# Optimization experiments

Hardware: AMD Instinct MI355X
Metric: run time of the kernel (lower is better)

Reference implementation:

```python
import jax, jax.numpy as jnp
import numpy as np

B, L = 2048, 64          # sentence pairs, leaves per balanced binary tree
V, IN, M, HID, NC = 50000, 300, 150, 50, 5


def setup_inputs() -> dict:
    key = jax.random.key(0)
    ks = jax.random.split(key, 16)
    lin = lambda k, fi, fo: jax.random.normal(k, (fi, fo), jnp.float32) / np.sqrt(fi).astype(np.float32)
    bias = lambda k, fo: jax.random.normal(k, (fo,), jnp.float32) * 0.01
    return {
        "ltokens": jax.random.randint(ks[0], (B, L), 0, V, dtype=jnp.int32),
        "rtokens": jax.random.randint(ks[1], (B, L), 0, V, dtype=jnp.int32),
        "emb":   jax.random.normal(ks[2], (V, IN), jnp.float32),
        "Wioux": lin(ks[3], IN, 3 * M), "bioux": bias(ks[4], 3 * M),
        "Wiouh": lin(ks[5], M, 3 * M), "biouh": bias(ks[6], 3 * M),
        "Wfx":   lin(ks[7], IN, M),    "bfx":   bias(ks[8], M),
        "Wfh":   lin(ks[9], M, M),     "bfh":   bias(ks[10], M),
        "Wh":    lin(ks[11], 2 * M, HID), "bh": bias(ks[12], HID),
        "Wp":    lin(ks[13], HID, NC),    "bp": bias(ks[14], NC),
    }


def _split_iou(iou, m):
    return iou[..., :m], iou[..., m:2 * m], iou[..., 2 * m:]


def _encode(tokens, emb, Wioux, bioux, Wiouh, biouh, Wfh, bfh):
    m = Wfh.shape[0]
    x = emb[tokens]                                   # [B, L, IN]
    # Leaves: child_h = child_c = 0, so iouh contributes only its bias and fc = 0.
    iou = x @ Wioux + bioux + biouh                   # [B, L, 3M]
    i, o, u = _split_iou(iou, m)
    c = jax.nn.sigmoid(i) * jnp.tanh(u)
    h = jax.nn.sigmoid(o) * jnp.tanh(c)
    # Internal nodes level by level (inputs=None branch of node_forward).
    while h.shape[1] > 1:
        Bq, n, _ = h.shape
        ch = h.reshape(Bq, n // 2, 2, m)              # children h
        cc = c.reshape(Bq, n // 2, 2, m)              # children c
        iou = ch.sum(axis=2) @ Wiouh + biouh          # child-sum
        i, o, u = _split_iou(iou, m)
        f = jax.nn.sigmoid(ch @ Wfh + bfh)            # per-child forget gate
        c = jax.nn.sigmoid(i) * jnp.tanh(u) + (f * cc).sum(axis=2)
        h = jax.nn.sigmoid(o) * jnp.tanh(c)
    # ROOT in the original just passes its single child's state through.
    return h[:, 0]                                    # [B, M]


def reference(ltokens, rtokens, emb, Wioux, bioux, Wiouh, biouh, Wfx, bfx, Wfh, bfh, Wh, bh, Wp, bp):
    lh = _encode(ltokens, emb, Wioux, bioux, Wiouh, biouh, Wfh, bfh)
    rh = _encode(rtokens, emb, Wioux, bioux, Wiouh, biouh, Wfh, bfh)
    vec = jnp.concatenate([lh * rh, jnp.abs(lh - rh)], axis=-1)   # [B, 2M]
    mid = jax.nn.sigmoid(vec @ Wh + bh)
    return jax.nn.log_softmax(mid @ Wp + bp, axis=-1)             # [B, NC]
```

## Files before the change

kernel.cpp:

```cpp
#include <hip/hip_runtime.h>
#include <hip/hip_bf16.h>
#include <math.h>

constexpr int B_   = 2048;
constexpr int L_   = 64;
constexpr int V_   = 50000;
constexpr int IN_  = 300;
constexpr int M_   = 150;
constexpr int HID_ = 50;
constexpr int NC_  = 5;

constexpr int KP_  = 160;
constexpr int GN_  = 608;
constexpr int GNT_ = 19;
constexpr int GKC_ = 5;
constexpr int GCH_ = GN_ * 32;
constexpr int GQS_ = GN_ * 8;
constexpr int GN2_  = 640;
constexpr int GNT2_ = 10;
constexpr int GCH2_ = GN2_ * 32;
constexpr int GQS2_ = GN2_ * 8;
constexpr int LEAF_N  = 480;
constexpr int LEAF_NT = 15;
constexpr int LEAF_KC = 10;
constexpr int LEAF_CH = LEAF_N * 32;
constexpr int LEAF_QS = LEAF_N * 8;

typedef float f32x4  __attribute__((ext_vector_type(4)));
typedef short bf16x8 __attribute__((ext_vector_type(8)));
typedef short short4v __attribute__((ext_vector_type(4)));

__device__ __forceinline__ float rcp_f(float x) { return __builtin_amdgcn_rcpf(x); }
__device__ __forceinline__ float sgm(float x)   { return rcp_f(1.0f + __expf(-x)); }
__device__ __forceinline__ float tanh_f(float x){ return 1.0f - 2.0f * rcp_f(1.0f + __expf(2.0f * x)); }

__device__ __forceinline__ short f2bs(float f) {
    union { __hip_bfloat16 h; short s; } u; u.h = __float2bfloat16(f); return u.s;
}
__device__ __forceinline__ float bs2f(short s) {
    union { short s; __hip_bfloat16 h; } u; u.s = s; return __bfloat162float(u.h);
}

__device__ __forceinline__ void gl_lds16(const short* g, short* l) {
    __builtin_amdgcn_global_load_lds(
        (const __attribute__((address_space(1))) unsigned int*)g,
        (__attribute__((address_space(3))) unsigned int*)l, 16, 0, 0);
}

__global__ __launch_bounds__(256) void prep_kernel(
    const float* __restrict__ Wioux, const float* __restrict__ Wiouh,
    const float* __restrict__ Wfh, short* __restrict__ Bg,
    short* __restrict__ Bg2, short* __restrict__ Bx)
{
    const int tid = blockIdx.x * blockDim.x + threadIdx.x;
    const int nthr = gridDim.x * blockDim.x;
    const int tot1 = GKC_ * GCH_;
    for (int idx = tid; idx < tot1; idx += nthr) {
        const int kc = idx / GCH_;
        int rem = idx % GCH_;
        const int q = rem / GQS_; rem %= GQS_;
        const int n = rem / 8, j = rem % 8;
        const int k = kc * 32 + q * 8 + j;
        const int m = n >> 2, g = n & 3;
        float v = 0.0f;
        if (k < M_ && m < M_)
            v = (g < 3) ? Wiouh[k * 450 + g * 150 + m] : Wfh[k * M_ + m];
        Bg[idx] = f2bs(v);
    }
    const int tot2 = GKC_ * GCH2_;
    for (int idx = tid; idx < tot2; idx += nthr) {
        const int kc = idx / GCH2_;
        int rem = idx % GCH2_;
        const int q = rem / GQS2_; rem %= GQS2_;
        const int n = rem / 8, j = rem % 8;
        const int k = kc * 32 + q * 8 + j;
        const int m = n >> 2, g = n & 3;
        float v = 0.0f;
        if (k < M_ && m < M_)
            v = (g < 3) ? Wiouh[k * 450 + g * 150 + m] : Wfh[k * M_ + m];
        Bg2[idx] = f2bs(v);
    }
    const int tot3 = LEAF_KC * LEAF_CH;
    for (int idx = tid; idx < tot3; idx += nthr) {
        const int kc = idx / LEAF_CH;
        int rem = idx % LEAF_CH;
        const int q = rem / LEAF_QS; rem %= LEAF_QS;
        const int n = rem / 8, j = rem % 8;
        const int k = kc * 32 + q * 8 + j;
        float v = (k < IN_ && n < 450) ? Wioux[k * 450 + n] : 0.0f;
        Bx[idx] = f2bs(v);
    }
}

__global__ __launch_bounds__(512) void leaf_gemm(
    const float* __restrict__ emb, const short* __restrict__ Bx,
    const float* __restrict__ bioux, const float* __restrict__ biouh,
    short* __restrict__ LeafH, short* __restrict__ LeafC)
{
    __shared__ __align__(16) char smem[LEAF_CH * 2 + 64 * 64];
    short* Bs = (short*)smem;
    short* As = (short*)(smem + LEAF_CH * 2);
    float* Es = (float*)smem;

    const int t = threadIdx.x;
    const int row0 = blockIdx.x * 64;
    const int w = t >> 6, lane = t & 63;
    const int mt = w & 3, nt0 = (w >> 2) * LEAF_NT;
    const int lr = lane & 15, quad = lane >> 4;

    f32x4 acc[LEAF_NT];
    #pragma unroll
    for (int i = 0; i < LEAF_NT; i++) { acc[i][0] = 0; acc[i][1] = 0; acc[i][2] = 0; acc[i][3] = 0; }

    const int arow = t >> 3, apart = t & 7;
    const int av = row0 + arow;
    const int aq = apart >> 1, aj = (apart & 1) * 4;

    for (int kc = 0; kc < LEAF_KC; kc++) {
        const short* bsrc = Bx + (size_t)kc * LEAF_CH;
        #pragma unroll
        for (int i = 0; i < 3; i++)
            gl_lds16(bsrc + (i * 512 + t) * 8, Bs + (i * 512 + (t & ~63)) * 8);
        if (t < 384)
            gl_lds16(bsrc + (1536 + t) * 8, Bs + (1536 + (t & ~63)) * 8);
        {
            const int k0 = kc * 32 + apart * 4;
            float4 x = make_float4(0.f, 0.f, 0.f, 0.f);
            if (av < V_ && k0 < IN_) x = *(const float4*)&emb[(size_t)av * IN_ + k0];
            short4v s;
            s[0] = f2bs(x.x); s[1] = f2bs(x.y); s[2] = f2bs(x.z); s[3] = f2bs(x.w);
            *(short4v*)&As[aq * 512 + arow * 8 + aj] = s;
        }
        __syncthreads();
        bf16x8 a = *(const bf16x8*)&As[quad * 512 + (mt * 16 + lr) * 8];
        #pragma unroll
        for (int i = 0; i < LEAF_NT; i++) {
            bf16x8 b = *(const bf16x8*)&Bs[quad * LEAF_QS + ((nt0 + i) * 16 + lr) * 8];
            acc[i] = __builtin_amdgcn_mfma_f32_16x16x32_bf16(a, b, acc[i], 0, 0, 0);
        }
        __syncthreads();
    }

    for (int mc = 0; mc < 4; mc++) {
        if (mt == mc) {
            #pragma unroll
            for (int i = 0; i < LEAF_NT; i++) {
                const int col = (nt0 + i) * 16 + lr;
                #pragma unroll
                for (int r = 0; r < 4; r++) Es[(quad * 4 + r) * LEAF_N + col] = acc[i][r];
            }
        }
        __syncthreads();
        for (int p = t; p < 16 * KP_; p += 512) {
            const int rl = p / KP_, n = p % KP_;
            const int v = row0 + mc * 16 + rl;
            if (v < V_) {
                if (n < M_) {
                    const float i_ = Es[rl * LEAF_N + n]       + bioux[n]       + biouh[n];
                    const float o_ = Es[rl * LEAF_N + n + 150] + bioux[n + 150] + biouh[n + 150];
                    const float u_ = Es[rl * LEAF_N + n + 300] + bioux[n + 300] + biouh[n + 300];
                    const float c = sgm(i_) * tanh_f(u_);
                    const float h = sgm(o_) * tanh_f(c);
                    LeafH[(size_t)v * KP_ + n] = f2bs(h);
                    LeafC[(size_t)v * KP_ + n] = f2bs(c);
                } else {
                    LeafH[(size_t)v * KP_ + n] = 0;
                    LeafC[(size_t)v * KP_ + n] = 0;
                }
            }
        }
        __syncthreads();
    }
}

__global__ __launch_bounds__(1024) void leafGF_gemm(
    const short* __restrict__ LeafH, const short* __restrict__ LeafC,
    const short* __restrict__ Bg2, const float* __restrict__ bfh,
    short* __restrict__ LeafE)
{
    __shared__ __align__(16) char smem[GCH2_ * 2 + 4096 + KP_ * 64 * 2 + 600];
    short* Bs   = (short*)smem;
    short* As   = (short*)(smem + GCH2_ * 2);
    short* CinS = (short*)(smem + GCH2_ * 2 + 4096);
    float* bfs  = (float*)(smem + GCH2_ * 2 + 4096 + KP_ * 64 * 2);
    short* Os = (short*)smem;

    const int t = threadIdx.x;
    const int v0 = blockIdx.x * 64;
    const int w = t >> 6, lane = t & 63;
    const int mt = w & 3, nt0 = (w >> 2) * GNT2_;
    const int lr = lane & 15, quad = lane >> 4;
    const int c = lane & 15;

    if (t < 150) bfs[t] = bfh[t];
    const short* csrc = LeafC + (size_t)v0 * KP_;
    gl_lds16(csrc + t * 8, CinS + (t & ~63) * 8);
    if (t < 256)
        gl_lds16(csrc + (1024 + t) * 8, CinS + (1024 + (t & ~63)) * 8);

    f32x4 acc[GNT2_];
    #pragma unroll
    for (int i = 0; i < GNT2_; i++) { acc[i][0] = 0; acc[i][1] = 0; acc[i][2] = 0; acc[i][3] = 0; }

    const int arow = t & 63, apart = t >> 6;
    const size_t srow = (size_t)((v0 + arow < V_) ? (v0 + arow) : 0);
    const short* asrc = LeafH + srow * KP_ + apart * 8;

    for (int kc = 0; kc < GKC_; kc++) {
        const short* bsrc = Bg2 + (size_t)kc * GCH2_;
        #pragma unroll
        for (int i = 0; i < 2; i++)
            gl_lds16(bsrc + (i * 1024 + t) * 8, Bs + (i * 1024 + (t & ~63)) * 8);
        if (t < 512)
            gl_lds16(bsrc + (2048 + t) * 8, Bs + (2048 + (t & ~63)) * 8);
        if (t < 256)
            gl_lds16(asrc + kc * 32, As + (t & ~63) * 8);
        __syncthreads();
        bf16x8 a = *(const bf16x8*)&As[quad * 512 + (mt * 16 + lr) * 8];
        #pragma unroll
        for (int i = 0; i < GNT2_; i++) {
            bf16x8 b = *(const bf16x8*)&Bs[quad * GQS2_ + ((nt0 + i) * 16 + lr) * 8];
            acc[i] = __builtin_amdgcn_mfma_f32_16x16x32_bf16(a, b, acc[i], 0, 0, 0);
        }
        __syncthreads();
    }

    for (int ph = 0; ph < 2; ph++) {
        if ((mt >> 1) == ph) {
            const int rbase = 16 * (mt & 1) + 4 * quad;
            #pragma unroll
            for (int i = 0; i < GNT2_; i++) {
                const int col = (nt0 + i) * 16 + c;
                if (col < GN_) {
                    const int m = col >> 2, g = col & 3;
                    #pragma unroll
                    for (int r = 0; r < 4; r++) {
                        short ov;
                        if (g == 3) {
                            if (m < M_) {
                                const float cc = bs2f(CinS[(32 * ph + rbase + r) * KP_ + m]);
                                ov = f2bs(sgm(acc[i][r] + bfs[m]) * cc);
                            } else ov = 0;
                        } else ov = f2bs(acc[i][r]);
                        Os[(rbase + r) * GN_ + col] = ov;
                    }
                }
            }
        }
        __syncthreads();
        const int vb = v0 + 32 * ph;
        const int4* os4 = (const int4*)Os;
        for (int u = t; u < 2432; u += 1024) {
            const int row = u / 76;
            if (vb + row < V_)
                ((int4*)(LeafE + (size_t)(vb + row) * GN_))[u - row * 76] = os4[u];
        }
        __syncthreads();
    }
}

template<int CS, int TNT>
__device__ __forceinline__ void level_epilogue(
    const f32x4* acc, int mt, int nt0, int lane,
    const short* CinS, const float* bias_s, short* Hs, short* Cs)
{
    const int q = lane >> 4, c = lane & 15, g = c & 3, lb = lane & ~3;
    #pragma unroll
    for (int i = 0; i < TNT; i++) {
        const int col = (nt0 + i) * 16 + c;
        const int m = col >> 2;
        const float vA = acc[i][0] + acc[i][1];
        const float vB = acc[i][2] + acc[i][3];
        const float iA = __shfl(vA, lb), oA = __shfl(vA, lb + 1), uA = __shfl(vA, lb + 2);
        const float iB = __shfl(vB, lb), oB = __shfl(vB, lb + 1), uB = __shfl(vB, lb + 2);
        const float fA0 = __shfl(acc[i][0], lb + 3), fA1 = __shfl(acc[i][1], lb + 3);
        const float fB0 = __shfl(acc[i][2], lb + 3), fB1 = __shfl(acc[i][3], lb + 3);
        if (g < 2 && m < M_) {
            const float iv = g ? iB : iA, ov = g ? oB : oA, uv = g ? uB : uA;
            const float fl = g ? fB0 : fA0, fr = g ? fB1 : fA1;
            const int node = 8 * mt + 2 * q + g;
            const int ch = 16 * mt + 4 * q + 2 * g;
            const float cl = bs2f(CinS[ch * CS + m]);
            const float cr = bs2f(CinS[(ch + 1) * CS + m]);
            const float bf = bias_s[450 + m];
            const float cv = sgm(iv + bias_s[m]) * tanh_f(uv + bias_s[m + 300])
                           + sgm(fl + bf) * cl + sgm(fr + bf) * cr;
            const float hv = sgm(ov + bias_s[m + 150]) * tanh_f(cv);
            Hs[node * KP_ + m] = f2bs(hv);
            Cs[node * KP_ + m] = f2bs(cv);
        }
    }
}

__global__ __launch_bounds__(512, 4) void level1_fused(
    const int* __restrict__ ltok, const int* __restrict__ rtok,
    const short* __restrict__ LeafE, const short* __restrict__ Bg,
    const float* __restrict__ biouh, const float* __restrict__ bfh,
    short* __restrict__ Hout, short* __restrict__ Cout)
{
    constexpr int CS1 = 152;
    __shared__ __align__(16) char smem[GCH_ * 2 + 20480 + 64 * CS1 * 2];
    short* Bs     = (short*)smem;
    short* AsF    = (short*)(smem + GCH_ * 2);
    short* CinS   = (short*)(smem + GCH_ * 2 + 20480);
    float* bias_s = (float*)(smem + 20480);
    short* Hs = Bs;
    short* Cs = Bs + 32 * KP_;

    const int t = threadIdx.x;
    const int out0 = blockIdx.x * 32;
    const int w = t >> 6, lane = t & 63;
    const int mt = w & 3, nt0 = (w >> 2) * GNT_;
    const int lr = lane & 15, quad = lane >> 4;

    if (t < 600) bias_s[t] = (t < 450) ? biouh[t] : bfh[t - 450];
    __syncthreads();

    {
        const int row = t >> 3, qs = t & 7;
        const int gidx = blockIdx.x * 128 + 2 * row;
        const int* tsrc = (gidx < B_ * L_) ? (ltok + gidx) : (rtok + gidx - B_ * L_);
        const short* el = LeafE + (size_t)tsrc[0] * GN_;
        const short* er = LeafE + (size_t)tsrc[1] * GN_;

        union U { int4 v[2]; short s16[16]; };
        U ue, ur, uen, urn;
        ue.v[0] = *(const int4*)(el + qs * 16);
        ue.v[1] = *(const int4*)(el + qs * 16 + 8);
        ur.v[0] = *(const int4*)(er + qs * 16);
        ur.v[1] = *(const int4*)(er + qs * 16 + 8);

        #pragma unroll 1
        for (int s = 0; s < 5; s++) {
            const int Q  = qs + 8 * s;
            const int Qn = Q + 8;
            if (s < 4 && Qn < 38) {
                uen.v[0] = *(const int4*)(el + Qn * 16);
                uen.v[1] = *(const int4*)(el + Qn * 16 + 8);
                urn.v[0] = *(const int4*)(er + Qn * 16);
                urn.v[1] = *(const int4*)(er + Qn * 16 + 8);
            }
            short4v hq = {0, 0, 0, 0}, cq = {0, 0, 0, 0};
            if (Q < 38) {
                #pragma unroll
                for (int jj = 0; jj < 4; jj++) {
                    const int m = 4 * Q + jj;
                    if (m < M_) {
                        const float i_ = bs2f(ue.s16[4 * jj])     + bs2f(ur.s16[4 * jj])     + bias_s[m];
                        const float o_ = bs2f(ue.s16[4 * jj + 1]) + bs2f(ur.s16[4 * jj + 1]) + bias_s[m + 150];
                        const float u_ = bs2f(ue.s16[4 * jj + 2]) + bs2f(ur.s16[4 * jj + 2]) + bias_s[m + 300];
                        const float fc = bs2f(ue.s16[4 * jj + 3]) + bs2f(ur.s16[4 * jj + 3]);
                        const float cv = sgm(i_) * tanh_f(u_) + fc;
                        const float hv = sgm(o_) * tanh_f(cv);
                        hq[jj] = f2bs(hv); cq[jj] = f2bs(cv);
                    }
                }
            }
            const int m0 = 4 * Q;
            const int kc = m0 >> 5, q = (m0 >> 3) & 3, j0 = m0 & 7;
            *(short4v*)&AsF[(kc * 4 + q) * 512 + row * 8 + j0] = hq;
            if (Q < 38)
                *(short4v*)&CinS[row * CS1 + m0] = cq;
            ue = uen; ur = urn;
        }
    }

    f32x4 acc[GNT_];
    #pragma unroll
    for (int i = 0; i < GNT_; i++) { acc[i][0] = 0; acc[i][1] = 0; acc[i][2] = 0; acc[i][3] = 0; }

    for (int kc = 0; kc < GKC_; kc++) {
        const short* bsrc = Bg + (size_t)kc * GCH_;
        #pragma unroll
        for (int i = 0; i < 4; i++)
            gl_lds16(bsrc + (i * 512 + t) * 8, Bs + (i * 512 + (t & ~63)) * 8);
        if (t < 384)
            gl_lds16(bsrc + (2048 + t) * 8, Bs + (2048 + (t & ~63)) * 8);
        __syncthreads();
        bf16x8 a = *(const bf16x8*)&AsF[kc * 2048 + quad * 512 + (mt * 16 + lr) * 8];
        #pragma unroll
        for (int i = 0; i < GNT_; i++) {
            bf16x8 b = *(const bf16x8*)&Bs[quad * GQS_ + ((nt0 + i) * 16 + lr) * 8];
            acc[i] = __builtin_amdgcn_mfma_f32_16x16x32_bf16(a, b, acc[i], 0, 0, 0);
        }
        __syncthreads();
    }

    if (t < 600) bias_s[t] = (t < 450) ? biouh[t] : bfh[t - 450];
    if (t < 320) { const int node = t / 10, mm = 150 + t % 10;
                   Hs[node * KP_ + mm] = 0; Cs[node * KP_ + mm] = 0; }
    __syncthreads();
    level_epilogue<CS1, GNT_>(acc, mt, nt0, lane, CinS, bias_s, Hs, Cs);
    __syncthreads();
    int4* Hg = (int4*)(Hout + (size_t)out0 * KP_);
    int4* Cg = (int4*)(Cout + (size_t)out0 * KP_);
    const int4* hs4 = (const int4*)Hs;
    const int4* cs4 = (const int4*)Cs;
    for (int u = t; u < 1280; u += 512) {
        if (u < 640) Hg[u] = hs4[u]; else Cg[u - 640] = cs4[u - 640];
    }
}

__global__ __launch_bounds__(1024) void level_gemm(
    const short* __restrict__ Hin, const short* __restrict__ Cin,
    const short* __restrict__ Bg2,
    const float* __restrict__ biouh, const float* __restrict__ bfh,
    short* __restrict__ Hout, short* __restrict__ Cout)
{
    __shared__ __align__(16) char smem[GCH2_ * 2 + 4096 + 20480 + 2400];
    short* Bs     = (short*)smem;
    short* As     = (short*)(smem + GCH2_ * 2);
    short* CinS   = (short*)(smem + GCH2_ * 2 + 4096);
    float* bias_s = (float*)(smem + GCH2_ * 2 + 4096 + 20480);
    short* Hs = Bs;
    short* Cs = Bs + 32 * KP_;

    const int t = threadIdx.x;
    const int row0 = blockIdx.x * 64, out0 = blockIdx.x * 32;
    const int w = t >> 6, lane = t & 63;
    const int mt = w & 3, nt0 = (w >> 2) * GNT2_;
    const int lr = lane & 15, quad = lane >> 4;

    if (t < 600) bias_s[t] = (t < 450) ? biouh[t] : bfh[t - 450];
    const short* csrc = Cin + (size_t)row0 * KP_;
    gl_lds16(csrc + t * 8, CinS + (t & ~63) * 8);
    if (t < 256)
        gl_lds16(csrc + (1024 + t) * 8, CinS + (1024 + (t & ~63)) * 8);

    f32x4 acc[GNT2_];
    #pragma unroll
    for (int i = 0; i < GNT2_; i++) { acc[i][0] = 0; acc[i][1] = 0; acc[i][2] = 0; acc[i][3] = 0; }

    const short* asrc = Hin + (size_t)(row0 + (t & 63)) * KP_ + (t >> 6) * 8;

    for (int kc = 0; kc < GKC_; kc++) {
        const short* bsrc = Bg2 + (size_t)kc * GCH2_;
        #pragma unroll
        for (int i = 0; i < 2; i++)
            gl_lds16(bsrc + (i * 1024 + t) * 8, Bs + (i * 1024 + (t & ~63)) * 8);
        if (t < 512)
            gl_lds16(bsrc + (2048 + t) * 8, Bs + (2048 + (t & ~63)) * 8);
        if (t < 256)
            gl_lds16(asrc + kc * 32, As + (t & ~63) * 8);
        __syncthreads();
        bf16x8 a = *(const bf16x8*)&As[quad * 512 + (mt * 16 + lr) * 8];
        #pragma unroll
        for (int i = 0; i < GNT2_; i++) {
            bf16x8 b = *(const bf16x8*)&Bs[quad * GQS2_ + ((nt0 + i) * 16 + lr) * 8];
            acc[i] = __builtin_amdgcn_mfma_f32_16x16x32_bf16(a, b, acc[i], 0, 0, 0);
        }
        __syncthreads();
    }

    if (t < 320) { const int node = t / 10, mm = 150 + t % 10;
                   Hs[node * KP_ + mm] = 0; Cs[node * KP_ + mm] = 0; }
    level_epilogue<KP_, GNT2_>(acc, mt, nt0, lane, CinS, bias_s, Hs, Cs);
    __syncthreads();
    int4* Hg = (int4*)(Hout + (size_t)out0 * KP_);
    int4* Cg = (int4*)(Cout + (size_t)out0 * KP_);
    const int4* hs4 = (const int4*)Hs;
    const int4* cs4 = (const int4*)Cs;
    for (int u = t; u < 1280; u += 1024) {
        if (u < 640) Hg[u] = hs4[u]; else Cg[u - 640] = cs4[u - 640];
    }
}

__global__ __launch_bounds__(64) void head_kernel(
    const short* __restrict__ RootH,
    const float* __restrict__ Wh, const float* __restrict__ bh,
    const float* __restrict__ Wp, const float* __restrict__ bp,
    float* __restrict__ out)
{
    __shared__ float vec[2 * M_];
    __shared__ float mid[HID_];
    __shared__ float lg[NC_];
    __shared__ float lse;

    const int b = blockIdx.x;
    const int t = threadIdx.x;
    const short* lh = RootH + (size_t)b * KP_;
    const short* rh = RootH + (size_t)(B_ + b) * KP_;

    for (int i = t; i < M_; i += 64) {
        const float a = bs2f(lh[i]), c = bs2f(rh[i]);
        vec[i]      = a * c;
        vec[M_ + i] = fabsf(a - c);
    }
    __syncthreads();

    for (int j = t; j < HID_; j += 64) {
        float acc = bh[j];
        for (int k = 0; k < 2 * M_; k++) acc += vec[k] * Wh[k * HID_ + j];
        mid[j] = sgm(acc);
    }
    __syncthreads();

    if (t < NC_) {
        float acc = bp[t];
        for (int k = 0; k < HID_; k++) acc += mid[k] * Wp[k * NC_ + t];
        lg[t] = acc;
    }
    __syncthreads();

    if (t == 0) {
        float mx = lg[0];
        for (int i = 1; i < NC_; i++) mx = fmaxf(mx, lg[i]);
        float s = 0.0f;
        for (int i = 0; i < NC_; i++) s += expf(lg[i] - mx);
        lse = mx + logf(s);
    }
    __syncthreads();

    if (t < NC_) out[b * NC_ + t] = lg[t] - lse;
}

extern "C" void kernel_launch(void* const* d_in, const int* in_sizes, int n_in,
                              void* d_out, int out_size, void* d_ws, size_t ws_size,
                              hipStream_t stream)
{
    const int*   ltok  = (const int*)d_in[0];
    const int*   rtok  = (const int*)d_in[1];
    const float* emb   = (const float*)d_in[2];
    const float* Wioux = (const float*)d_in[3];
    const float* bioux = (const float*)d_in[4];
    const float* Wiouh = (const float*)d_in[5];
    const float* biouh = (const float*)d_in[6];
    const float* Wfh   = (const float*)d_in[9];
    const float* bfh   = (const float*)d_in[10];
    const float* Wh    = (const float*)d_in[11];
    const float* bh    = (const float*)d_in[12];
    const float* Wp    = (const float*)d_in[13];
    const float* bp    = (const float*)d_in[14];
    float* out = (float*)d_out;

    char* ws = (char*)d_ws;
    size_t off = 0;
    auto carve = [&](size_t bytes) { char* p = ws + off; off += (bytes + 255) & ~(size_t)255; return p; };
    short* Bg    = (short*)carve((size_t)GKC_ * GCH_ * 2);
    short* Bg2   = (short*)carve((size_t)GKC_ * GCH2_ * 2);
    short* Bx    = (short*)carve((size_t)LEAF_KC * LEAF_CH * 2);
    short* LeafH = (short*)carve((size_t)V_ * KP_ * 2);
    short* LeafC = (short*)carve((size_t)V_ * KP_ * 2);
    short* LeafE = (short*)carve((size_t)V_ * GN_ * 2);
    short* HA    = (short*)carve((size_t)65536 * KP_ * 2);
    short* CA    = (short*)carve((size_t)65536 * KP_ * 2);
    short* HB    = (short*)carve((size_t)32768 * KP_ * 2);
    short* CB    = (short*)carve((size_t)32768 * KP_ * 2);

    hipLaunchKernelGGL(prep_kernel, dim3(128), dim3(256), 0, stream, Wioux, Wiouh, Wfh, Bg, Bg2, Bx);
    hipLaunchKernelGGL(leaf_gemm, dim3((V_ + 63) / 64), dim3(512), 0, stream,
                       emb, Bx, bioux, biouh, LeafH, LeafC);
    hipLaunchKernelGGL(leafGF_gemm, dim3((V_ + 63) / 64), dim3(1024), 0, stream,
                       LeafH, LeafC, Bg2, bfh, LeafE);
    hipLaunchKernelGGL(level1_fused, dim3(2048), dim3(512), 0, stream,
                       ltok, rtok, LeafE, Bg, biouh, bfh, HA, CA);
    hipLaunchKernelGGL(level_gemm, dim3(1024), dim3(1024), 0, stream,
                       HA, CA, Bg2, biouh, bfh, HB, CB);
    hipLaunchKernelGGL(level_gemm, dim3(512), dim3(1024), 0, stream,
                       HB, CB, Bg2, biouh, bfh, HA, CA);
    hipLaunchKernelGGL(level_gemm, dim3(256), dim3(1024), 0, stream,
                       HA, CA, Bg2, biouh, bfh, HB, CB);
    hipLaunchKernelGGL(level_gemm, dim3(128), dim3(1024), 0, stream,
                       HB, CB, Bg2, biouh, bfh, HA, CA);
    hipLaunchKernelGGL(head_kernel, dim3(B_), dim3(64), 0, stream, HA, Wh, bh, Wp, bp, out);
}
```

Baseline: 486.1 us.

## Split level1 GEMM into two N-halves and fold leaf biouh into LeafE

The level1_fused kernel now computes its 19 N-tiles in two passes of 10 and 9. After each pass the epilogue results are packed into registers, so the live accumulator set shrinks and register pressure under the 512x4 launch bounds is meant to drop. The B matrix is reloaded twice, and the shared-memory bias staging plus its barrier are removed. The i/o/u half-bias is folded into LeafE by leafGF_gemm, so the level1 prologue skips the bias adds. The cost is double B-chunk traffic and extra MFMA loop overhead, and bias values are now rounded to bf16.

Measured after the change: 492.0 us. Within noise of the previous version (+1.2%).

```diff
diff --git a/kernel.cpp b/kernel.cpp
--- a/kernel.cpp
+++ b/kernel.cpp
@@ -175,14 +175,14 @@
 
 __global__ __launch_bounds__(1024) void leafGF_gemm(
     const short* __restrict__ LeafH, const short* __restrict__ LeafC,
-    const short* __restrict__ Bg2, const float* __restrict__ bfh,
-    short* __restrict__ LeafE)
-{
-    __shared__ __align__(16) char smem[GCH2_ * 2 + 4096 + KP_ * 64 * 2 + 600];
-    short* Bs   = (short*)smem;
-    short* As   = (short*)(smem + GCH2_ * 2);
-    short* CinS = (short*)(smem + GCH2_ * 2 + 4096);
-    float* bfs  = (float*)(smem + GCH2_ * 2 + 4096 + KP_ * 64 * 2);
+    const short* __restrict__ Bg2, const float* __restrict__ biouh,
+    const float* __restrict__ bfh, short* __restrict__ LeafE)
+{
+    __shared__ __align__(16) char smem[GCH2_ * 2 + 4096 + KP_ * 64 * 2 + 2400];
+    short* Bs     = (short*)smem;
+    short* As     = (short*)(smem + GCH2_ * 2);
+    short* CinS   = (short*)(smem + GCH2_ * 2 + 4096);
+    float* bias_s = (float*)(smem + GCH2_ * 2 + 4096 + KP_ * 64 * 2);
     short* Os = (short*)smem;
 
     const int t = threadIdx.x;
@@ -192,7 +192,7 @@
     const int lr = lane & 15, quad = lane >> 4;
     const int c = lane & 15;
 
-    if (t < 150) bfs[t] = bfh[t];
+    if (t < 600) bias_s[t] = (t < 450) ? biouh[t] : bfh[t - 450];
     const short* csrc = LeafC + (size_t)v0 * KP_;
     gl_lds16(csrc + t * 8, CinS + (t & ~63) * 8);
     if (t < 256)
@@ -239,9 +239,13 @@
                         if (g == 3) {
                             if (m < M_) {
                                 const float cc = bs2f(CinS[(32 * ph + rbase + r) * KP_ + m]);
-                                ov = f2bs(sgm(acc[i][r] + bfs[m]) * cc);
+                                ov = f2bs(sgm(acc[i][r] + bias_s[450 + m]) * cc);
                             } else ov = 0;
-                        } else ov = f2bs(acc[i][r]);
+                        } else {
+                            float gv = acc[i][r];
+                            if (m < M_) gv += 0.5f * bias_s[g * 150 + m];
+                            ov = f2bs(gv);
+                        }
                         Os[(rbase + r) * GN_ + col] = ov;
                     }
                 }
@@ -292,6 +296,58 @@
     }
 }
 
+template<int T0, int TN>
+__device__ __forceinline__ void epi_half_pack(
+    const f32x4* acc, int mt, int nt0, int lane, const short* CinS,
+    const float* __restrict__ biouh, const float* __restrict__ bfh,
+    unsigned int* pack)
+{
+    const int q = lane >> 4, c = lane & 15, g = c & 3, lb = lane & ~3;
+    #pragma unroll
+    for (int i = 0; i < TN; i++) {
+        const int col = (nt0 + T0 + i) * 16 + c;
+        const int m = col >> 2;
+        const float vA = acc[i][0] + acc[i][1];
+        const float vB = acc[i][2] + acc[i][3];
+        const float iA = __shfl(vA, lb), oA = __shfl(vA, lb + 1), uA = __shfl(vA, lb + 2);
+        const float iB = __shfl(vB, lb), oB = __shfl(vB, lb + 1), uB = __shfl(vB, lb + 2);
+        const float fA0 = __shfl(acc[i][0], lb + 3), fA1 = __shfl(acc[i][1], lb + 3);
+        const float fB0 = __shfl(acc[i][2], lb + 3), fB1 = __shfl(acc[i][3], lb + 3);
+        unsigned int pk = 0;
+        if (g < 2 && m < M_) {
+            const float iv = g ? iB : iA, ov = g ? oB : oA, uv = g ? uB : uA;
+            const float fl = g ? fB0 : fA0, fr = g ? fB1 : fA1;
+            const int ch = 16 * mt + 4 * q + 2 * g;
+            const float cl = bs2f(CinS[ch * 152 + m]);
+            const float cr = bs2f(CinS[(ch + 1) * 152 + m]);
+            const float bf = bfh[m];
+            const float cv = sgm(iv + biouh[m]) * tanh_f(uv + biouh[m + 300])
+                           + sgm(fl + bf) * cl + sgm(fr + bf) * cr;
+            const float hv = sgm(ov + biouh[m + 150]) * tanh_f(cv);
+            pk = ((unsigned int)(unsigned short)f2bs(hv) << 16)
+               |  (unsigned int)(unsigned short)f2bs(cv);
+        }
+        pack[i] = pk;
+    }
+}
+
+template<int T0, int TN>
+__device__ __forceinline__ void unpack_half(
+    const unsigned int* pack, int mt, int nt0, int lane, short* Hs, short* Cs)
+{
+    const int q = lane >> 4, c = lane & 15, g = c & 3;
+    #pragma unroll
+    for (int i = 0; i < TN; i++) {
+        const int col = (nt0 + T0 + i) * 16 + c;
+        const int m = col >> 2;
+        if (g < 2 && m < M_) {
+            const int node = 8 * mt + 2 * q + g;
+            Hs[node * KP_ + m] = (short)(pack[i] >> 16);
+            Cs[node * KP_ + m] = (short)(pack[i] & 0xffff);
+        }
+    }
+}
+
 __global__ __launch_bounds__(512, 4) void level1_fused(
     const int* __restrict__ ltok, const int* __restrict__ rtok,
     const short* __restrict__ LeafE, const short* __restrict__ Bg,
@@ -303,7 +359,6 @@
     short* Bs     = (short*)smem;
     short* AsF    = (short*)(smem + GCH_ * 2);
     short* CinS   = (short*)(smem + GCH_ * 2 + 20480);
-    float* bias_s = (float*)(smem + 20480);
     short* Hs = Bs;
     short* Cs = Bs + 32 * KP_;
 
@@ -312,9 +367,6 @@
     const int w = t >> 6, lane = t & 63;
     const int mt = w & 3, nt0 = (w >> 2) * GNT_;
     const int lr = lane & 15, quad = lane >> 4;
-
-    if (t < 600) bias_s[t] = (t < 450) ? biouh[t] : bfh[t - 450];
-    __syncthreads();
 
     {
         const int row = t >> 3, qs = t & 7;
@@ -346,9 +398,9 @@
                 for (int jj = 0; jj < 4; jj++) {
                     const int m = 4 * Q + jj;
                     if (m < M_) {
-                        const float i_ = bs2f(ue.s16[4 * jj])     + bs2f(ur.s16[4 * jj])     + bias_s[m];
-                        const float o_ = bs2f(ue.s16[4 * jj + 1]) + bs2f(ur.s16[4 * jj + 1]) + bias_s[m + 150];
-                        const float u_ = bs2f(ue.s16[4 * jj + 2]) + bs2f(ur.s16[4 * jj + 2]) + bias_s[m + 300];
+                        const float i_ = bs2f(ue.s16[4 * jj])     + bs2f(ur.s16[4 * jj]);
+                        const float o_ = bs2f(ue.s16[4 * jj + 1]) + bs2f(ur.s16[4 * jj + 1]);
+                        const float u_ = bs2f(ue.s16[4 * jj + 2]) + bs2f(ur.s16[4 * jj + 2]);
                         const float fc = bs2f(ue.s16[4 * jj + 3]) + bs2f(ur.s16[4 * jj + 3]);
                         const float cv = sgm(i_) * tanh_f(u_) + fc;
                         const float hv = sgm(o_) * tanh_f(cv);
@@ -365,10 +417,11 @@
         }
     }
 
-    f32x4 acc[GNT_];
-    #pragma unroll
-    for (int i = 0; i < GNT_; i++) { acc[i][0] = 0; acc[i][1] = 0; acc[i][2] = 0; acc[i][3] = 0; }
-
+    unsigned int packA[10], packB[9];
+    f32x4 acc[10];
+
+    #pragma unroll
+    for (int i = 0; i < 10; i++) { acc[i][0] = 0; acc[i][1] = 0; acc[i][2] = 0; acc[i][3] = 0; }
     for (int kc = 0; kc < GKC_; kc++) {
         const short* bsrc = Bg + (size_t)kc * GCH_;
         #pragma unroll
@@ -379,18 +432,38 @@
         __syncthreads();
         bf16x8 a = *(const bf16x8*)&AsF[kc * 2048 + quad * 512 + (mt * 16 + lr) * 8];
         #pragma unroll
-        for (int i = 0; i < GNT_; i++) {
+        for (int i = 0; i < 10; i++) {
             bf16x8 b = *(const bf16x8*)&Bs[quad * GQS_ + ((nt0 + i) * 16 + lr) * 8];
             acc[i] = __builtin_amdgcn_mfma_f32_16x16x32_bf16(a, b, acc[i], 0, 0, 0);
         }
         __syncthreads();
     }
-
-    if (t < 600) bias_s[t] = (t < 450) ? biouh[t] : bfh[t - 450];
+    epi_half_pack<0, 10>(acc, mt, nt0, lane, CinS, biouh, bfh, packA);
+
+    #pragma unroll
+    for (int i = 0; i < 9; i++) { acc[i][0] = 0; acc[i][1] = 0; acc[i][2] = 0; acc[i][3] = 0; }
+    for (int kc = 0; kc < GKC_; kc++) {
+        const short* bsrc = Bg + (size_t)kc * GCH_;
+        #pragma unroll
+        for (int i = 0; i < 4; i++)
+            gl_lds16(bsrc + (i * 512 + t) * 8, Bs + (i * 512 + (t & ~63)) * 8);
+        if (t < 384)
+            gl_lds16(bsrc + (2048 + t) * 8, Bs + (2048 + (t & ~63)) * 8);
+        __syncthreads();
+        bf16x8 a = *(const bf16x8*)&AsF[kc * 2048 + quad * 512 + (mt * 16 + lr) * 8];
+        #pragma unroll
+        for (int i = 0; i < 9; i++) {
+            bf16x8 b = *(const bf16x8*)&Bs[quad * GQS_ + ((nt0 + 10 + i) * 16 + lr) * 8];
+            acc[i] = __builtin_amdgcn_mfma_f32_16x16x32_bf16(a, b, acc[i], 0, 0, 0);
+        }
+        __syncthreads();
+    }
+    epi_half_pack<10, 9>(acc, mt, nt0, lane, CinS, biouh, bfh, packB);
+
     if (t < 320) { const int node = t / 10, mm = 150 + t % 10;
                    Hs[node * KP_ + mm] = 0; Cs[node * KP_ + mm] = 0; }
-    __syncthreads();
-    level_epilogue<CS1, GNT_>(acc, mt, nt0, lane, CinS, bias_s, Hs, Cs);
+    unpack_half<0, 10>(packA, mt, nt0, lane, Hs, Cs);
+    unpack_half<10, 9>(packB, mt, nt0, lane, Hs, Cs);
     __syncthreads();
     int4* Hg = (int4*)(Hout + (size_t)out0 * KP_);
     int4* Cg = (int4*)(Cout + (size_t)out0 * KP_);
@@ -551,7 +624,7 @@
     hipLaunchKernelGGL(leaf_gemm, dim3((V_ + 63) / 64), dim3(512), 0, stream,
                        emb, Bx, bioux, biouh, LeafH, LeafC);
     hipLaunchKernelGGL(leafGF_gemm, dim3((V_ + 63) / 64), dim3(1024), 0, stream,
-                       LeafH, LeafC, Bg2, bfh, LeafE);
+                       LeafH, LeafC, Bg2, biouh, bfh, LeafE);
     hipLaunchKernelGGL(level1_fused, dim3(2048), dim3(512), 0, stream,
                        ltok, rtok, LeafE, Bg, biouh, bfh, HA, CA);
     hipLaunchKernelGGL(level_gemm, dim3(1024), dim3(1024), 0, stream,
```
